# Optimization experiments

Measured on AMD Instinct MI355X. Metric: run time of the kernel, lower is better.

Reference implementation:

```python
import jax, jax.numpy as jnp
import numpy as np

ALPHA = 1.0


def setup_inputs() -> dict:
    key = jax.random.key(0)
    k1, k2 = jax.random.split(key)
    B, K, D = 65536, 256, 768
    embeddings = jax.random.normal(k1, (B, D), dtype=jnp.float32)
    centroids = jax.random.normal(k2, (K, D), dtype=jnp.float32)
    return {"embeddings": embeddings, "centroids": centroids}


def reference(embeddings, centroids):
    # Batched L2 cdist via the (|e|^2 + |c|^2 - 2 e.c) expansion; avoids the
    # per-sample Python loop in the original and never materializes [B,K,D].
    e2 = jnp.sum(embeddings * embeddings, axis=-1, keepdims=True)      # [B,1]
    c2 = jnp.sum(centroids * centroids, axis=-1)                       # [K]
    d2 = e2 + c2[None, :] - 2.0 * (embeddings @ centroids.T)          # [B,K]
    dist = jnp.sqrt(jnp.maximum(d2, 0.0))                              # [B,K]

    predicted_labels = jnp.argmin(dist, axis=1)                        # [B]

    # Faithful to source: transpose to [K,B]; softmin is over the BATCH axis
    # per centroid, and the final mean is over centroids.
    dT = dist.T                                                        # [K,B]
    minv = jnp.min(dT, axis=1, keepdims=True)                          # [K,1]
    exps = jnp.exp(-ALPHA * (dT - minv))                               # [K,B]
    softmin = exps / jnp.sum(exps, axis=1, keepdims=True)              # [K,B]
    clustering_loss = jnp.mean(jnp.sum(dT * softmin, axis=1))          # scalar

    return clustering_loss, predicted_labels
```

## Files before the change

### kernel.cpp

```cpp
#include <hip/hip_runtime.h>
#include <math.h>
#include <float.h>

#define D_DIM 768
#define K_C   256
#define KC    32
#define NCH   24
#define BMR   256
#define NTHR  1024
#define MARGIN 1.5e-2f
#define M0SHIFT 39.0f

typedef __attribute__((ext_vector_type(8))) short s16x8;
typedef __attribute__((ext_vector_type(4))) float f32x4;

__device__ inline unsigned short f2bf(float x) {
    unsigned u = __float_as_uint(x);
    unsigned r = 0x7FFFu + ((u >> 16) & 1u);
    return (unsigned short)((u + r) >> 16);
}
__device__ inline int swz(int row, int slot) {
    return row*32 + (((slot ^ (row >> 1)) & 3) << 3);
}
__device__ inline void gl_lds16(const void* g, void* l) {
    __builtin_amdgcn_global_load_lds(
        (const __attribute__((address_space(1))) void*)g,
        (__attribute__((address_space(3))) void*)l, 16, 0, 0);
}
__device__ inline unsigned pk2(float a, float b) {
    return __builtin_amdgcn_perm(__float_as_uint(b), __float_as_uint(a), 0x07060302u);
}

__global__ __launch_bounds__(256) void kprep(const float* __restrict__ C,
    short* __restrict__ Cimg, float* __restrict__ c2f,
    float* __restrict__ g1, float* __restrict__ g2, int* __restrict__ done)
{
    const int k = blockIdx.x;
    const int t = threadIdx.x;
    __shared__ double red[4];
    double s = 0.0;
#pragma unroll
    for (int i = 0; i < 3; ++i) {
        int d = t + 256*i;
        float x = C[(size_t)k*D_DIM + d];
        s += (double)x * (double)x;
        int ch = d >> 5, g = (d & 31) >> 3, e = d & 7;
        Cimg[(size_t)ch*8192 + swz(k, g) + e] = (short)f2bf(x);
    }
#pragma unroll
    for (int m = 1; m < 64; m <<= 1) s += __shfl_xor(s, m, 64);
    if ((t & 63) == 0) red[t >> 6] = s;
    __syncthreads();
    if (t == 0) {
        c2f[k] = (float)(red[0] + red[1] + red[2] + red[3]);
        g1[k] = 0.f; g2[k] = 0.f;
        if (k == 0) *done = 0;
    }
}

#define ECONV_M(Q0,Q1,EHI) do {                                         \
        e2p = fmaf(Q0.x,Q0.x,e2p); e2p = fmaf(Q0.y,Q0.y,e2p);           \
        e2p = fmaf(Q0.z,Q0.z,e2p); e2p = fmaf(Q0.w,Q0.w,e2p);           \
        e2p = fmaf(Q1.x,Q1.x,e2p); e2p = fmaf(Q1.y,Q1.y,e2p);           \
        e2p = fmaf(Q1.z,Q1.z,e2p); e2p = fmaf(Q1.w,Q1.w,e2p);           \
        uint4 Ha;                                                       \
        Ha.x = pk2(Q0.x,Q0.y); Ha.y = pk2(Q0.z,Q0.w);                   \
        Ha.z = pk2(Q1.x,Q1.y); Ha.w = pk2(Q1.z,Q1.w);                   \
        *reinterpret_cast<uint4*>((EHI) + ebyte) = Ha;                  \
    } while (0)

#define MFMA_M(EB,CB) do {                                              \
        s16x8 ah_[4];                                                   \
        _Pragma("unroll")                                               \
        for (int m_ = 0; m_ < 4; ++m_)                                  \
            ah_[m_] = *reinterpret_cast<const s16x8*>((EB) + aoff[m_]); \
        _Pragma("unroll")                                               \
        for (int n_ = 0; n_ < 4; ++n_) {                                \
            s16x8 bh_ = *reinterpret_cast<const s16x8*>((CB) + boff[n_]); \
            _Pragma("unroll")                                           \
            for (int m_ = 0; m_ < 4; ++m_)                              \
                acc[m_][n_] = __builtin_amdgcn_mfma_f32_16x16x32_bf16(ah_[m_], bh_, acc[m_][n_], 0, 0, 0); \
        }                                                               \
    } while (0)

#define CSTAGE_M(CHI,DST) do {                                          \
        const char* img_ = (const char*)Cimg + (size_t)(CHI)*16384;     \
        gl_lds16(img_ + t*16, (DST) + t*16);                            \
    } while (0)

#define WAITBAR(N) do {                                                 \
        asm volatile("s_waitcnt vmcnt(" #N ") lgkmcnt(0)" ::: "memory");\
        __builtin_amdgcn_s_barrier();                                   \
        __builtin_amdgcn_sched_barrier(0);                              \
    } while (0)

#define EQLOAD(QV0,QV1,CHI) do {                                        \
        const float* ep_ = Ep + (CHI)*KC;                               \
        QV0 = *reinterpret_cast<const float4*>(ep_);                    \
        QV1 = *reinterpret_cast<const float4*>(ep_ + 4);                \
    } while (0)

__global__ __launch_bounds__(NTHR, 4) void kdist(const float* __restrict__ E,
    const float* __restrict__ Cf, const short* __restrict__ Cimg,
    const float* __restrict__ c2f, float* __restrict__ labels,
    float* __restrict__ g1, float* __restrict__ g2,
    int* __restrict__ done, float* __restrict__ out)
{
    __shared__ __align__(16) char lds[65536];
    float*  e2s   = (float*)lds;
    float*  spart = (float*)(lds + 1024);
    float4* topb  = (float4*)(lds + 9216);
    int*    qcnt  = (int*)(lds + 25600);
    int4*   qlist = (int4*)(lds + 25616);
    int*    lastf = (int*)(lds + 29712);
    float*  fred  = (float*)(lds + 29728);

    const int t    = threadIdx.x;
    const int lane = t & 63;
    const int w    = t >> 6;
    const int wm   = w >> 2, wn = w & 3;
    const int c4   = lane & 15, sgr = lane >> 4;
    const int R0   = blockIdx.x * BMR;

    f32x4 acc[4][4];
#pragma unroll
    for (int m = 0; m < 4; ++m)
#pragma unroll
        for (int n = 0; n < 4; ++n) acc[m][n] = (f32x4){0.f,0.f,0.f,0.f};

    const int erow = t >> 2, eseg = t & 3;
    const float* Ep = E + (size_t)(R0 + erow)*D_DIM + eseg*8;
    const int ebyte = 2*swz(erow, eseg);
    int aoff[4], boff[4];
#pragma unroll
    for (int m = 0; m < 4; ++m) aoff[m] = 2*swz(wm*64 + m*16 + c4, sgr);
#pragma unroll
    for (int n = 0; n < 4; ++n) boff[n] = 2*swz(wn*64 + n*16 + c4, sgr);
    float e2p = 0.f;
    float4 qa0, qa1, qb0, qb1;

    CSTAGE_M(0, lds + 32768);
    __builtin_amdgcn_sched_barrier(0);
    EQLOAD(qa0, qa1, 0);
    ECONV_M(qa0, qa1, lds);
    EQLOAD(qb0, qb1, 1);
    asm volatile("s_waitcnt lgkmcnt(0)" ::: "memory");
    __builtin_amdgcn_s_barrier();
    __builtin_amdgcn_sched_barrier(0);

#pragma unroll 1
    for (int pr = 0; pr < 11; ++pr) {
        const int ch = 2*pr;
        CSTAGE_M(ch + 1, lds + 49152);
        __builtin_amdgcn_sched_barrier(0);
        EQLOAD(qa0, qa1, ch + 2);
        MFMA_M(lds, lds + 32768);
        ECONV_M(qb0, qb1, lds + 16384);
        WAITBAR(2);
        CSTAGE_M(ch + 2, lds + 32768);
        __builtin_amdgcn_sched_barrier(0);
        EQLOAD(qb0, qb1, ch + 3);
        MFMA_M(lds + 16384, lds + 49152);
        ECONV_M(qa0, qa1, lds);
        WAITBAR(2);
    }
    CSTAGE_M(23, lds + 49152);
    __builtin_amdgcn_sched_barrier(0);
    MFMA_M(lds, lds + 32768);
    ECONV_M(qb0, qb1, lds + 16384);
    WAITBAR(0);
    MFMA_M(lds + 16384, lds + 49152);
    __syncthreads();

    {
        float es = e2p + __shfl_xor(e2p, 1, 64);
        es += __shfl_xor(es, 2, 64);
        if ((t & 3) == 0) e2s[t >> 2] = es;
        if (t == 0) *qcnt = 0;
    }
    __syncthreads();

    float e2r[4][4];
#pragma unroll
    for (int m = 0; m < 4; ++m)
#pragma unroll
        for (int g = 0; g < 4; ++g)
            e2r[m][g] = e2s[wm*64 + m*16 + sgr*4 + g];
    float c2v[4];
#pragma unroll
    for (int n = 0; n < 4; ++n) c2v[n] = c2f[wn*64 + n*16 + c4];

#pragma unroll
    for (int m = 0; m < 4; ++m)
#pragma unroll
        for (int n = 0; n < 4; ++n) {
            f32x4 v = acc[m][n];
#pragma unroll
            for (int g = 0; g < 4; ++g) {
                float d2 = fmaf(-2.f, v[g], e2r[m][g] + c2v[n]);
                v[g] = sqrtf(fmaxf(d2, 0.f));
            }
            acc[m][n] = v;
        }

#pragma unroll
    for (int m = 0; m < 4; ++m)
#pragma unroll
        for (int g = 0; g < 4; ++g) {
            float k1 = FLT_MAX, k2 = FLT_MAX, k3 = FLT_MAX;
#pragma unroll
            for (int n = 0; n < 4; ++n) {
                unsigned idx = (unsigned)(wn*64 + n*16 + c4);
                unsigned u = __float_as_uint(acc[m][n][g]);
                float kd = __uint_as_float(((u - idx + 127u) & 0xFFFFFF00u) | idx);
                if (kd < k1)      { k3 = k2; k2 = k1; k1 = kd; }
                else if (kd < k2) { k3 = k2; k2 = kd; }
                else if (kd < k3) { k3 = kd; }
            }
#pragma unroll
            for (int msk = 1; msk < 16; msk <<= 1) {
                float o1 = __shfl_xor(k1, msk, 64);
                float o2 = __shfl_xor(k2, msk, 64);
                float o3 = __shfl_xor(k3, msk, 64);
                float m1 = fminf(k1, o1), M1 = fmaxf(k1, o1);
                float m2 = fminf(k2, o2), M2 = fmaxf(k2, o2);
                float r3 = fminf(k3, o3);
                k1 = m1;
                k2 = fminf(M1, m2);
                k3 = fminf(fmaxf(M1, m2), fminf(M2, r3));
            }
            if (c4 == 0)
                topb[wn*BMR + wm*64 + m*16 + sgr*4 + g] = (float4){k1, k2, k3, 0.f};
        }

#pragma unroll
    for (int n = 0; n < 4; ++n) {
        float s1 = 0.f, s2 = 0.f;
#pragma unroll
        for (int m = 0; m < 4; ++m)
#pragma unroll
            for (int g = 0; g < 4; ++g) {
                float d = acc[m][n][g];
                float wgt = __expf(M0SHIFT - d);
                s1 += wgt; s2 = fmaf(d, wgt, s2);
            }
        s1 += __shfl_xor(s1, 16, 64); s2 += __shfl_xor(s2, 16, 64);
        s1 += __shfl_xor(s1, 32, 64); s2 += __shfl_xor(s2, 32, 64);
        if (lane < 16) {
            int cc = wn*64 + n*16 + c4;
            float* p = &spart[(size_t)(wm*K_C + cc)*2];
            p[0] = s1; p[1] = s2;
        }
    }
    __syncthreads();

    if (t < BMR) {
        float4 q0 = topb[t],           q1 = topb[BMR + t];
        float4 q2 = topb[2*BMR + t],   q3 = topb[3*BMR + t];
#define MRG3(A1,A2,A3,B1,B2,B3,R1,R2,R3) do {                           \
        float m1_ = fminf(A1,B1), M1_ = fmaxf(A1,B1);                   \
        float m2_ = fminf(A2,B2), M2_ = fmaxf(A2,B2);                   \
        float r3_ = fminf(A3,B3);                                       \
        R1 = m1_; R2 = fminf(M1_, m2_);                                 \
        R3 = fminf(fmaxf(M1_, m2_), fminf(M2_, r3_)); } while (0)
        float a1, a2, a3, b1, b2, b3, k1, k2, k3;
        MRG3(q0.x,q0.y,q0.z, q1.x,q1.y,q1.z, a1,a2,a3);
        MRG3(q2.x,q2.y,q2.z, q3.x,q3.y,q3.z, b1,b2,b3);
        MRG3(a1,a2,a3, b1,b2,b3, k1,k2,k3);
#undef MRG3
        unsigned u1 = __float_as_uint(k1), u2 = __float_as_uint(k2), u3 = __float_as_uint(k3);
        int i1 = (int)(u1 & 255u), i2 = (int)(u2 & 255u), i3 = (int)(u3 & 255u);
        float v1 = __uint_as_float(u1 & 0xFFFFFF00u);
        float v2 = __uint_as_float(u2 & 0xFFFFFF00u);
        int row = R0 + t;
        labels[row] = (float)i1;
        if (v2 - v1 < MARGIN) {
            int slot = atomicAdd(qcnt, 1);
            qlist[slot] = make_int4(row, i1, i2, i3);
        }
    }
    if (t < K_C) {
        float s1 = 0.f, s2 = 0.f;
#pragma unroll
        for (int q = 0; q < 4; ++q) {
            s1 += spart[(size_t)(q*K_C + t)*2];
            s2 += spart[(size_t)(q*K_C + t)*2 + 1];
        }
        atomicAdd(&g1[t], s1);
        atomicAdd(&g2[t], s2);
    }
    __syncthreads();

    const int nq = *qcnt;
    for (int e = w; e < nq; e += 16) {
        int4 q = qlist[e];
        const int row = q.x, k1 = q.y, k2 = q.z, k3 = q.w;
        double s1 = 0, s2 = 0, s3 = 0;
#pragma unroll 1
        for (int d = lane; d < D_DIM; d += 64) {
            double ed = (double)E[(size_t)row*D_DIM + d];
            double ca = (double)Cf[(size_t)k1*D_DIM + d];
            double cb = (double)Cf[(size_t)k2*D_DIM + d];
            double cc = (double)Cf[(size_t)k3*D_DIM + d];
            s1 += ca*(ca - 2.0*ed);
            s2 += cb*(cb - 2.0*ed);
            s3 += cc*(cc - 2.0*ed);
        }
#pragma unroll
        for (int msk = 32; msk; msk >>= 1) {
            s1 += __shfl_down(s1, msk, 64);
            s2 += __shfl_down(s2, msk, 64);
            s3 += __shfl_down(s3, msk, 64);
        }
        if (lane == 0) {
            double bv = s1; int bk = k1;
            if (s2 < bv || (s2 == bv && k2 < bk)) { bv = s2; bk = k2; }
            if (s3 < bv || (s3 == bv && k3 < bk)) { bv = s3; bk = k3; }
            labels[row] = (float)bk;
        }
    }

    __syncthreads();
    if (t == 0) {
        __threadfence();
        *lastf = (atomicAdd(done, 1) == (int)gridDim.x - 1) ? 1 : 0;
    }
    __syncthreads();
    if (*lastf) {
        float v = 0.f;
        if (t < K_C) {
            float a = atomicAdd(&g1[t], 0.f);
            float b = atomicAdd(&g2[t], 0.f);
            v = b / a;
        }
#pragma unroll
        for (int msk = 1; msk < 64; msk <<= 1) v += __shfl_xor(v, msk, 64);
        if (lane == 0 && w < 4) fred[w] = v;
        __syncthreads();
        if (t == 0) out[0] = (fred[0] + fred[1] + fred[2] + fred[3]) / 256.0f;
    }
}

extern "C" void kernel_launch(void* const* d_in, const int* in_sizes, int n_in,
                              void* d_out, int out_size, void* d_ws, size_t ws_size,
                              hipStream_t stream)
{
    const float* E = (const float*)d_in[0];
    const float* C = (const float*)d_in[1];
    float* out = (float*)d_out;

    const int Bn = in_sizes[0] / D_DIM;
    const int NB = Bn / BMR;

    char* ws = (char*)d_ws;
    float* c2f  = (float*)ws;
    float* g1   = (float*)(ws + 1024);
    float* g2   = (float*)(ws + 2048);
    int*   done = (int*)(ws + 3072);
    short* Cimg = (short*)(ws + 4096);
    float* labels = out + 1;

    kprep <<<K_C, 256, 0, stream>>>(C, Cimg, c2f, g1, g2, done);
    kdist <<<NB,  NTHR, 0, stream>>>(E, C, Cimg, c2f, labels, g1, g2, done, out);
}
```

Before: 80.20 us.

## Double-buffer two K-chunks per stage in enlarged LDS, halving barriers

```diff
diff --git a/kernel.cpp b/kernel.cpp
--- a/kernel.cpp
+++ b/kernel.cpp
@@ -88,12 +88,6 @@
         gl_lds16(img_ + t*16, (DST) + t*16);                            \
     } while (0)
 
-#define WAITBAR(N) do {                                                 \
-        asm volatile("s_waitcnt vmcnt(" #N ") lgkmcnt(0)" ::: "memory");\
-        __builtin_amdgcn_s_barrier();                                   \
-        __builtin_amdgcn_sched_barrier(0);                              \
-    } while (0)
-
 #define EQLOAD(QV0,QV1,CHI) do {                                        \
         const float* ep_ = Ep + (CHI)*KC;                               \
         QV0 = *reinterpret_cast<const float4*>(ep_);                    \
@@ -106,7 +100,7 @@
     float* __restrict__ g1, float* __restrict__ g2,
     int* __restrict__ done, float* __restrict__ out)
 {
-    __shared__ __align__(16) char lds[65536];
+    __shared__ __align__(16) char lds[131072];
     float*  e2s   = (float*)lds;
     float*  spart = (float*)(lds + 1024);
     float4* topb  = (float4*)(lds + 9216);
@@ -139,37 +133,40 @@
     float e2p = 0.f;
     float4 qa0, qa1, qb0, qb1;
 
-    CSTAGE_M(0, lds + 32768);
+    CSTAGE_M(0, lds + 65536);
+    CSTAGE_M(1, lds + 65536 + 16384);
     __builtin_amdgcn_sched_barrier(0);
     EQLOAD(qa0, qa1, 0);
+    EQLOAD(qb0, qb1, 1);
     ECONV_M(qa0, qa1, lds);
-    EQLOAD(qb0, qb1, 1);
+    ECONV_M(qb0, qb1, lds + 16384);
     asm volatile("s_waitcnt lgkmcnt(0)" ::: "memory");
     __builtin_amdgcn_s_barrier();
     __builtin_amdgcn_sched_barrier(0);
 
 #pragma unroll 1
     for (int pr = 0; pr < 11; ++pr) {
-        const int ch = 2*pr;
-        CSTAGE_M(ch + 1, lds + 49152);
+        const int cur = pr & 1;
+        char* ecur = lds + (cur << 15);
+        char* enxt = lds + ((1 - cur) << 15);
+        char* ccur = lds + 65536 + (cur << 15);
+        char* cnxt = lds + 65536 + ((1 - cur) << 15);
+        const int ch = 2*pr + 2;
+        CSTAGE_M(ch,     cnxt);
+        CSTAGE_M(ch + 1, cnxt + 16384);
         __builtin_amdgcn_sched_barrier(0);
-        EQLOAD(qa0, qa1, ch + 2);
-        MFMA_M(lds, lds + 32768);
-        ECONV_M(qb0, qb1, lds + 16384);
-        WAITBAR(2);
-        CSTAGE_M(ch + 2, lds + 32768);
+        EQLOAD(qa0, qa1, ch);
+        EQLOAD(qb0, qb1, ch + 1);
+        MFMA_M(ecur, ccur);
+        MFMA_M(ecur + 16384, ccur + 16384);
+        ECONV_M(qa0, qa1, enxt);
+        ECONV_M(qb0, qb1, enxt + 16384);
+        asm volatile("s_waitcnt lgkmcnt(0)" ::: "memory");
+        __builtin_amdgcn_s_barrier();
         __builtin_amdgcn_sched_barrier(0);
-        EQLOAD(qb0, qb1, ch + 3);
-        MFMA_M(lds + 16384, lds + 49152);
-        ECONV_M(qa0, qa1, lds);
-        WAITBAR(2);
-    }
-    CSTAGE_M(23, lds + 49152);
-    __builtin_amdgcn_sched_barrier(0);
-    MFMA_M(lds, lds + 32768);
-    ECONV_M(qb0, qb1, lds + 16384);
-    WAITBAR(0);
-    MFMA_M(lds + 16384, lds + 49152);
+    }
+    MFMA_M(lds + 32768,         lds + 98304);
+    MFMA_M(lds + 32768 + 16384, lds + 98304 + 16384);
     __syncthreads();
 
     {
```

New measurement: 85.41 us. 6.5% more time.
